# Kernel tuning notes

Hardware: AMD Instinct MI355X
Metric: run time of the kernel (lower is better)

The kernel has to match this reference:

```python
import jax, jax.numpy as jnp
import numpy as np

D_MODEL = 1024
NHEAD = 16
HEAD_DIM = D_MODEL // NHEAD
LN_EPS = 1e-5
ROPE_BASE = 10000.0


def _rope_cos_sin(n, head_dim):
    inv_freq = 1.0 / (ROPE_BASE ** (jnp.arange(0, head_dim, 2, dtype=jnp.float32) / head_dim))
    t = jnp.arange(n, dtype=jnp.float32)
    freqs = jnp.outer(t, inv_freq)  # (N, head_dim//2)
    return jnp.cos(freqs), jnp.sin(freqs)


def _apply_rope(x, cos, sin):
    # x: (B, H, N, hd); cos/sin: (N, hd//2)
    B, H, N, hd = x.shape
    xr = x.reshape(B, H, N, hd // 2, 2)
    x0, x1 = xr[..., 0], xr[..., 1]
    c = cos[None, None]
    s = sin[None, None]
    rot = jnp.stack([x0 * c - x1 * s, x0 * s + x1 * c], axis=-1)
    return rot.reshape(B, H, N, hd)


def setup_inputs() -> dict:
    key = jax.random.key(0)
    ks = jax.random.split(key, 6)
    D = D_MODEL
    scale = 1.0 / np.sqrt(D)
    x = jax.random.normal(ks[0], (2, 2048, D), dtype=jnp.float32)
    Wq = jax.random.normal(ks[1], (D, D), dtype=jnp.float32) * scale
    Wk = jax.random.normal(ks[2], (D, D), dtype=jnp.float32) * scale
    Wv = jax.random.normal(ks[3], (D, D), dtype=jnp.float32) * scale
    Wo = jax.random.normal(ks[4], (D, D), dtype=jnp.float32) * scale
    bq = jnp.zeros((D,), jnp.float32)
    bk = jnp.zeros((D,), jnp.float32)
    bv = jnp.zeros((D,), jnp.float32)
    bo = jnp.zeros((D,), jnp.float32)
    ln_w = jnp.ones((D,), jnp.float32)
    ln_b = jnp.zeros((D,), jnp.float32)
    return {"x": x, "ln_w": ln_w, "ln_b": ln_b, "Wq": Wq, "bq": bq,
            "Wk": Wk, "bk": bk, "Wv": Wv, "bv": bv, "Wo": Wo, "bo": bo}


def reference(x, ln_w, ln_b, Wq, bq, Wk, bk, Wv, bv, Wo, bo):
    B, N, D = x.shape
    H, hd = NHEAD, HEAD_DIM
    # LayerNorm
    mu = jnp.mean(x, axis=-1, keepdims=True)
    var = jnp.mean(jnp.square(x - mu), axis=-1, keepdims=True)
    xn = (x - mu) * jax.lax.rsqrt(var + LN_EPS) * ln_w + ln_b
    # QKV projections -> (B, H, N, hd)
    def proj(W, b):
        return (xn @ W.T + b).reshape(B, N, H, hd).transpose(0, 2, 1, 3)
    q = proj(Wq, bq)
    k = proj(Wk, bk)
    v = proj(Wv, bv)
    cos, sin = _rope_cos_sin(N, hd)
    q = _apply_rope(q, cos, sin)
    k = _apply_rope(k, cos, sin)
    scores = jnp.einsum('bhqd,bhkd->bhqk', q, k) / jnp.sqrt(jnp.float32(hd))
    attn = jax.nn.softmax(scores, axis=-1)
    out = jnp.einsum('bhqk,bhkd->bhqd', attn, v)
    out = out.transpose(0, 2, 1, 3).reshape(B, N, D)
    return x + out @ Wo.T + bo
```

## Files before the change

kernel.cpp:

```cpp
#include <hip/hip_runtime.h>


#define SEQ 2048
#define LN_EPS 1e-5f

using short8 = __attribute__((ext_vector_type(8))) short;
using f32x4  = __attribute__((ext_vector_type(4))) float;

__device__ __forceinline__ unsigned short f2bf(float f) {
  union { float f; unsigned u; } v; v.f = f;
  unsigned r = v.u + 0x7FFFu + ((v.u >> 16) & 1u);
  return (unsigned short)(r >> 16);
}

__device__ __forceinline__ void async16(const void* g, void* l) {
  __builtin_amdgcn_global_load_lds(
      (const __attribute__((address_space(1))) void*)g,
      (__attribute__((address_space(3))) void*)l, 16, 0, 0);
}

__global__ __launch_bounds__(256) void prep_kernel(
    const float* __restrict__ x, const float* __restrict__ lnw, const float* __restrict__ lnb,
    const float* __restrict__ wq, const float* __restrict__ wk,
    const float* __restrict__ wv, const float* __restrict__ wo,
    unsigned short* __restrict__ wqkv, unsigned short* __restrict__ wob,
    unsigned short* __restrict__ xn, float2* __restrict__ tab) {
  const int b = blockIdx.x, t = threadIdx.x;
  if (b < 4096) {
    const int gid = b * 256 + t;
    const int m = gid >> 18, e4 = gid & 262143;
    const float* src = (m == 0) ? wq : (m == 1) ? wk : (m == 2) ? wv : wo;
    const float4 v = ((const float4*)src)[e4];
    ushort4 o; o.x = f2bf(v.x); o.y = f2bf(v.y); o.z = f2bf(v.z); o.w = f2bf(v.w);
    if (m < 3) ((ushort4*)wqkv)[(size_t)m * 262144 + e4] = o;
    else       ((ushort4*)wob)[e4] = o;
  } else if (b < 8192) {
    const int row = b - 4096;
    const float4 v = ((const float4*)(x + (size_t)row * 1024))[t];
    float s  = v.x + v.y + v.z + v.w;
    float s2 = v.x * v.x + v.y * v.y + v.z * v.z + v.w * v.w;
#pragma unroll
    for (int off = 32; off >= 1; off >>= 1) {
      s  += __shfl_xor(s, off);
      s2 += __shfl_xor(s2, off);
    }
    __shared__ float red[8];
    const int lane = t & 63, wave = t >> 6;
    if (lane == 0) { red[wave] = s; red[4 + wave] = s2; }
    __syncthreads();
    s  = red[0] + red[1] + red[2] + red[3];
    s2 = red[4] + red[5] + red[6] + red[7];
    const float mu   = s * (1.0f / 1024.0f);
    const float var  = s2 * (1.0f / 1024.0f) - mu * mu;
    const float rstd = rsqrtf(var + LN_EPS);
    const float4 wv4 = ((const float4*)lnw)[t];
    const float4 bv4 = ((const float4*)lnb)[t];
    ushort4 o;
    o.x = f2bf((v.x - mu) * rstd * wv4.x + bv4.x);
    o.y = f2bf((v.y - mu) * rstd * wv4.y + bv4.y);
    o.z = f2bf((v.z - mu) * rstd * wv4.z + bv4.z);
    o.w = f2bf((v.w - mu) * rstd * wv4.w + bv4.w);
    ((ushort4*)xn)[(size_t)row * 256 + t] = o;
  } else {
    const int gid = (b - 8192) * 256 + t;
    const int pos = gid >> 5, ip = gid & 31;
    const float invf = exp2f((float)ip * -0.4152410118609203f);
    const float fr = (float)pos * invf;
    tab[gid] = make_float2(cosf(fr), sinf(fr));
  }
}

__global__ __launch_bounds__(256, 3) void gemm_kernel(
    const unsigned short* __restrict__ A,
    const unsigned short* __restrict__ Bw,
    int mode,
    const float* __restrict__ bq, const float* __restrict__ bk, const float* __restrict__ bv,
    const float2* __restrict__ tab,
    unsigned short* __restrict__ qb, unsigned short* __restrict__ kbg,
    unsigned short* __restrict__ vtb,
    const float* __restrict__ bo, const float* __restrict__ xres, float* __restrict__ out) {
  __shared__ unsigned short lA[128 * 64];
  __shared__ unsigned short lB[128 * 64];
  const int tid = threadIdx.x;
  const int lane = tid & 63, wave = tid >> 6;
  const int lr = lane & 15, quad = lane >> 4;
  const int wm = (wave >> 1) * 64, wn = (wave & 1) * 64;
  const int n0 = blockIdx.x * 128, m0 = blockIdx.y * 128;
  const int r7 = lr & 7;
  const int lrow = lane >> 3, lcg = (lane & 7) ^ lrow;

  f32x4 acc[4][4];
#pragma unroll
  for (int i = 0; i < 4; ++i)
#pragma unroll
    for (int j = 0; j < 4; ++j) acc[i][j] = (f32x4){0.f, 0.f, 0.f, 0.f};

  for (int kt = 0; kt < 16; ++kt) {
    __syncthreads();
#pragma unroll
    for (int c = 0; c < 4; ++c) {
      const int chunk = wave * 4 + c;
      const int grow = chunk * 8 + lrow;
      async16(&A[(size_t)(m0 + grow) * 1024 + kt * 64 + lcg * 8], &lA[chunk * 512]);
      async16(&Bw[(size_t)(n0 + grow) * 1024 + kt * 64 + lcg * 8], &lB[chunk * 512]);
    }
    __syncthreads();
#pragma unroll
    for (int kk = 0; kk < 2; ++kk) {
      short8 a[4], b[4];
#pragma unroll
      for (int i = 0; i < 4; ++i)
        a[i] = *(const short8*)&lA[(wm + i * 16 + lr) * 64 + ((kk * 4 + quad) ^ r7) * 8];
#pragma unroll
      for (int j = 0; j < 4; ++j)
        b[j] = *(const short8*)&lB[(wn + j * 16 + lr) * 64 + ((kk * 4 + quad) ^ r7) * 8];
#pragma unroll
      for (int i = 0; i < 4; ++i)
#pragma unroll
        for (int j = 0; j < 4; ++j)
          acc[i][j] = __builtin_amdgcn_mfma_f32_16x16x32_bf16(a[i], b[j], acc[i][j], 0, 0, 0);
    }
  }

  if (mode == 0) {
    const int which = n0 >> 10;
    const float* bias = (which == 0) ? bq : (which == 1) ? bk : bv;
    const float qs = (which == 0) ? 0.18033688011112042f : 1.0f;
#pragma unroll
    for (int i = 0; i < 4; ++i)
#pragma unroll
      for (int j = 0; j < 4; ++j)
#pragma unroll
        for (int r = 0; r < 4; ++r) {
          const int row = m0 + wm + i * 16 + quad * 4 + r;
          const int col = n0 + wn + j * 16 + lr;
          const int c = col & 1023;
          float val = (acc[i][j][r] + bias[c]) * qs;
          const int head = c >> 6, hd_i = c & 63;
          const int b_ = row >> 11, pos = row & 2047;
          if (which < 2) {
            const float partner = __shfl_xor(val, 1);
            const float2 cs = tab[(pos << 5) + (hd_i >> 1)];
            val = val * cs.x + partner * ((lane & 1) ? cs.y : -cs.y);
          }
          if (which == 2) {
            vtb[((size_t)((b_ * 16 + head) * 64 + hd_i)) * SEQ + pos] = f2bf(val);
          } else {
            const size_t didx = ((size_t)((b_ * 16 + head) * SEQ + pos)) * 64 + hd_i;
            if (which == 0) qb[didx] = f2bf(val);
            else            kbg[didx] = f2bf(val);
          }
        }
  } else {
#pragma unroll
    for (int i = 0; i < 4; ++i)
#pragma unroll
      for (int j = 0; j < 4; ++j)
#pragma unroll
        for (int r = 0; r < 4; ++r) {
          const int row = m0 + wm + i * 16 + quad * 4 + r;
          const int col = n0 + wn + j * 16 + lr;
          const size_t idx = (size_t)row * 1024 + col;
          out[idx] = acc[i][j][r] + bo[col] + xres[idx];
        }
  }
}

__global__ __launch_bounds__(256) void attn_kernel(
    const unsigned short* __restrict__ qg, const unsigned short* __restrict__ kg,
    const unsigned short* __restrict__ vtg, unsigned short* __restrict__ ao) {
  __shared__ unsigned short lK[64 * 64];
  __shared__ unsigned short lV[64 * 64];
  __shared__ unsigned short lP[128 * 72];
  const int tid = threadIdx.x;
  const int lane = tid & 63, w = tid >> 6;
  const int lr = lane & 15, quad = lane >> 4;
  const int r7 = lr & 7;
  const int lrow = lane >> 3, lcg = (lane & 7) ^ lrow;
  const int bh = blockIdx.x >> 4, qt = blockIdx.x & 15;
  const int q0 = qt * 128 + w * 32;
  const unsigned short* Q  = qg + (size_t)bh * SEQ * 64;
  const unsigned short* K  = kg + (size_t)bh * SEQ * 64;
  const unsigned short* VT = vtg + (size_t)bh * 64 * SEQ;

  short8 qf[2][2];
#pragma unroll
  for (int t = 0; t < 2; ++t)
#pragma unroll
    for (int kk = 0; kk < 2; ++kk)
      qf[t][kk] = *(const short8*)&Q[(size_t)(q0 + t * 16 + lr) * 64 + kk * 32 + quad * 8];

  short8 onesf;
  {
    const short o1 = (lr == 0) ? (short)0x3F80 : (short)0;
#pragma unroll
    for (int j = 0; j < 8; ++j) onesf[j] = o1;
  }

  f32x4 o[2][4], ol[2];
#pragma unroll
  for (int t = 0; t < 2; ++t) {
    ol[t] = (f32x4){0.f, 0.f, 0.f, 0.f};
#pragma unroll
    for (int d = 0; d < 4; ++d) o[t][d] = (f32x4){0.f, 0.f, 0.f, 0.f};
  }

  for (int kt = 0; kt < 32; ++kt) {
    __syncthreads();
#pragma unroll
    for (int c = 0; c < 2; ++c) {
      const int chunk = w * 2 + c;
      const int row = chunk * 8 + lrow;
      async16(&K[(size_t)(kt * 64 + row) * 64 + lcg * 8], &lK[chunk * 512]);
      async16(&VT[(size_t)row * SEQ + kt * 64 + lcg * 8], &lV[chunk * 512]);
    }
    __syncthreads();

#pragma unroll
    for (int kb = 0; kb < 4; ++kb) {
      const short8 k0 = *(const short8*)&lK[(kb * 16 + lr) * 64 + (quad ^ r7) * 8];
      const short8 k1 = *(const short8*)&lK[(kb * 16 + lr) * 64 + ((4 + quad) ^ r7) * 8];
#pragma unroll
      for (int t = 0; t < 2; ++t) {
        f32x4 st = (f32x4){0.f, 0.f, 0.f, 0.f};
        st = __builtin_amdgcn_mfma_f32_16x16x32_bf16(k0, qf[t][0], st, 0, 0, 0);
        st = __builtin_amdgcn_mfma_f32_16x16x32_bf16(k1, qf[t][1], st, 0, 0, 0);
        union { float f; unsigned u; } c0, c1, c2, c3;
        c0.f = __builtin_amdgcn_exp2f(st[0]);
        c1.f = __builtin_amdgcn_exp2f(st[1]);
        c2.f = __builtin_amdgcn_exp2f(st[2]);
        c3.f = __builtin_amdgcn_exp2f(st[3]);
        uint2 pw;
        pw.x = __builtin_amdgcn_perm(c1.u, c0.u, 0x07060302u);
        pw.y = __builtin_amdgcn_perm(c3.u, c2.u, 0x07060302u);
        *(uint2*)&lP[(w * 32 + t * 16 + lr) * 72 + kb * 16 + quad * 4] = pw;
      }
    }
    __asm__ __volatile__("s_waitcnt lgkmcnt(0)" ::: "memory");

#pragma unroll
    for (int k2 = 0; k2 < 2; ++k2) {
      const short8 pf0 = *(const short8*)&lP[(w * 32 + lr) * 72 + k2 * 32 + quad * 8];
      const short8 pf1 = *(const short8*)&lP[(w * 32 + 16 + lr) * 72 + k2 * 32 + quad * 8];
      ol[0] = __builtin_amdgcn_mfma_f32_16x16x32_bf16(pf0, onesf, ol[0], 0, 0, 0);
      ol[1] = __builtin_amdgcn_mfma_f32_16x16x32_bf16(pf1, onesf, ol[1], 0, 0, 0);
#pragma unroll
      for (int d = 0; d < 4; ++d) {
        const short8 vf = *(const short8*)&lV[(d * 16 + lr) * 64 + ((k2 * 4 + quad) ^ r7) * 8];
        o[0][d] = __builtin_amdgcn_mfma_f32_16x16x32_bf16(pf0, vf, o[0][d], 0, 0, 0);
        o[1][d] = __builtin_amdgcn_mfma_f32_16x16x32_bf16(pf1, vf, o[1][d], 0, 0, 0);
      }
    }
  }

  const int b_ = bh >> 4, h = bh & 15;
#pragma unroll
  for (int t = 0; t < 2; ++t)
#pragma unroll
    for (int r = 0; r < 4; ++r) {
      const float l = __shfl(ol[t][r], lane & 48);
      const float rl = 1.0f / l;
#pragma unroll
      for (int d = 0; d < 4; ++d) {
        const int row = q0 + t * 16 + quad * 4 + r;
        ao[(size_t)(b_ * SEQ + row) * 1024 + h * 64 + d * 16 + lr] = f2bf(o[t][d][r] * rl);
      }
    }
}

extern "C" void kernel_launch(void* const* d_in, const int* in_sizes, int n_in,
                              void* d_out, int out_size, void* d_ws, size_t ws_size,
                              hipStream_t stream) {
  const float* x   = (const float*)d_in[0];
  const float* lnw = (const float*)d_in[1];
  const float* lnb = (const float*)d_in[2];
  const float* Wq  = (const float*)d_in[3];
  const float* bq  = (const float*)d_in[4];
  const float* Wk  = (const float*)d_in[5];
  const float* bk  = (const float*)d_in[6];
  const float* Wv  = (const float*)d_in[7];
  const float* bv  = (const float*)d_in[8];
  const float* Wo  = (const float*)d_in[9];
  const float* bo  = (const float*)d_in[10];
  float* out = (float*)d_out;

  char* ws = (char*)d_ws;
  unsigned short* wqkv = (unsigned short*)(ws);
  unsigned short* wob  = (unsigned short*)(ws + 6291456);
  unsigned short* xn   = (unsigned short*)(ws + 8388608);
  unsigned short* qb   = (unsigned short*)(ws + 16777216);
  unsigned short* kbuf = (unsigned short*)(ws + 25165824);
  unsigned short* vtb  = (unsigned short*)(ws + 33554432);
  unsigned short* ao   = (unsigned short*)(ws + 41943040);
  float2*         tab  = (float2*)(ws + 50331648);

  hipLaunchKernelGGL(prep_kernel, dim3(8448), dim3(256), 0, stream,
                     x, lnw, lnb, Wq, Wk, Wv, Wo, wqkv, wob, xn, tab);
  hipLaunchKernelGGL(gemm_kernel, dim3(24, 32), dim3(256), 0, stream,
                     xn, wqkv, 0, bq, bk, bv, tab, qb, kbuf, vtb,
                     (const float*)nullptr, (const float*)nullptr, (float*)nullptr);
  hipLaunchKernelGGL(attn_kernel, dim3(512), dim3(256), 0, stream, qb, kbuf, vtb, ao);
  hipLaunchKernelGGL(gemm_kernel, dim3(8, 32), dim3(256), 0, stream,
                     ao, wob, 1,
                     (const float*)nullptr, (const float*)nullptr, (const float*)nullptr, tab,
                     (unsigned short*)nullptr, (unsigned short*)nullptr, (unsigned short*)nullptr,
                     bo, x, out);
}
```

Baseline: 222.6 us.

## Drop LDS staging; load GEMM and attention MFMA fragments directly from global

The QKV GEMM, output GEMM and attention kernels stop staging tiles in shared memory with async global-to-LDS copies and block barriers. Each wave now reads its MFMA operand fragments straight from global memory through precomputed row pointers and relies on cache hits for reuse across waves. The single GEMM kernel is split into a QKV kernel and an output-projection kernel; the latter uses narrower 64-column tiles, which doubles the block count. Attention keeps only a per-wave swizzled P buffer in LDS and adds a redundant zero store before each P write. This removes barrier and LDS traffic but gives up explicit tile sharing, so it risks more global/L2 traffic and exposed load latency.

After: 370.3 us. +66.4%, slower.

```diff
diff --git a/kernel.cpp b/kernel.cpp
--- a/kernel.cpp
+++ b/kernel.cpp
@@ -11,12 +11,6 @@
   union { float f; unsigned u; } v; v.f = f;
   unsigned r = v.u + 0x7FFFu + ((v.u >> 16) & 1u);
   return (unsigned short)(r >> 16);
-}
-
-__device__ __forceinline__ void async16(const void* g, void* l) {
-  __builtin_amdgcn_global_load_lds(
-      (const __attribute__((address_space(1))) void*)g,
-      (__attribute__((address_space(3))) void*)l, 16, 0, 0);
 }
 
 __global__ __launch_bounds__(256) void prep_kernel(
@@ -70,24 +64,26 @@
   }
 }
 
-__global__ __launch_bounds__(256, 3) void gemm_kernel(
+__global__ __launch_bounds__(256, 3) void gemm_qkv_kernel(
     const unsigned short* __restrict__ A,
     const unsigned short* __restrict__ Bw,
-    int mode,
     const float* __restrict__ bq, const float* __restrict__ bk, const float* __restrict__ bv,
     const float2* __restrict__ tab,
     unsigned short* __restrict__ qb, unsigned short* __restrict__ kbg,
-    unsigned short* __restrict__ vtb,
-    const float* __restrict__ bo, const float* __restrict__ xres, float* __restrict__ out) {
-  __shared__ unsigned short lA[128 * 64];
-  __shared__ unsigned short lB[128 * 64];
+    unsigned short* __restrict__ vtb) {
   const int tid = threadIdx.x;
   const int lane = tid & 63, wave = tid >> 6;
   const int lr = lane & 15, quad = lane >> 4;
   const int wm = (wave >> 1) * 64, wn = (wave & 1) * 64;
   const int n0 = blockIdx.x * 128, m0 = blockIdx.y * 128;
-  const int r7 = lr & 7;
-  const int lrow = lane >> 3, lcg = (lane & 7) ^ lrow;
+
+  const unsigned short* ap[4];
+  const unsigned short* bp[4];
+#pragma unroll
+  for (int i = 0; i < 4; ++i) {
+    ap[i] = &A[(size_t)(m0 + wm + i * 16 + lr) * 1024 + quad * 8];
+    bp[i] = &Bw[(size_t)(n0 + wn + i * 16 + lr) * 1024 + quad * 8];
+  }
 
   f32x4 acc[4][4];
 #pragma unroll
@@ -96,24 +92,14 @@
     for (int j = 0; j < 4; ++j) acc[i][j] = (f32x4){0.f, 0.f, 0.f, 0.f};
 
   for (int kt = 0; kt < 16; ++kt) {
-    __syncthreads();
-#pragma unroll
-    for (int c = 0; c < 4; ++c) {
-      const int chunk = wave * 4 + c;
-      const int grow = chunk * 8 + lrow;
-      async16(&A[(size_t)(m0 + grow) * 1024 + kt * 64 + lcg * 8], &lA[chunk * 512]);
-      async16(&Bw[(size_t)(n0 + grow) * 1024 + kt * 64 + lcg * 8], &lB[chunk * 512]);
-    }
-    __syncthreads();
 #pragma unroll
     for (int kk = 0; kk < 2; ++kk) {
+      const int off = kt * 64 + kk * 32;
       short8 a[4], b[4];
 #pragma unroll
-      for (int i = 0; i < 4; ++i)
-        a[i] = *(const short8*)&lA[(wm + i * 16 + lr) * 64 + ((kk * 4 + quad) ^ r7) * 8];
-#pragma unroll
-      for (int j = 0; j < 4; ++j)
-        b[j] = *(const short8*)&lB[(wn + j * 16 + lr) * 64 + ((kk * 4 + quad) ^ r7) * 8];
+      for (int i = 0; i < 4; ++i) a[i] = *(const short8*)(ap[i] + off);
+#pragma unroll
+      for (int j = 0; j < 4; ++j) b[j] = *(const short8*)(bp[j] + off);
 #pragma unroll
       for (int i = 0; i < 4; ++i)
 #pragma unroll
@@ -122,66 +108,105 @@
     }
   }
 
-  if (mode == 0) {
-    const int which = n0 >> 10;
-    const float* bias = (which == 0) ? bq : (which == 1) ? bk : bv;
-    const float qs = (which == 0) ? 0.18033688011112042f : 1.0f;
-#pragma unroll
-    for (int i = 0; i < 4; ++i)
-#pragma unroll
-      for (int j = 0; j < 4; ++j)
-#pragma unroll
-        for (int r = 0; r < 4; ++r) {
-          const int row = m0 + wm + i * 16 + quad * 4 + r;
-          const int col = n0 + wn + j * 16 + lr;
-          const int c = col & 1023;
-          float val = (acc[i][j][r] + bias[c]) * qs;
-          const int head = c >> 6, hd_i = c & 63;
-          const int b_ = row >> 11, pos = row & 2047;
-          if (which < 2) {
-            const float partner = __shfl_xor(val, 1);
-            const float2 cs = tab[(pos << 5) + (hd_i >> 1)];
-            val = val * cs.x + partner * ((lane & 1) ? cs.y : -cs.y);
-          }
-          if (which == 2) {
-            vtb[((size_t)((b_ * 16 + head) * 64 + hd_i)) * SEQ + pos] = f2bf(val);
-          } else {
-            const size_t didx = ((size_t)((b_ * 16 + head) * SEQ + pos)) * 64 + hd_i;
-            if (which == 0) qb[didx] = f2bf(val);
-            else            kbg[didx] = f2bf(val);
-          }
+  const int which = n0 >> 10;
+  const float* bias = (which == 0) ? bq : (which == 1) ? bk : bv;
+  const float qs = (which == 0) ? 0.18033688011112042f : 1.0f;
+#pragma unroll
+  for (int i = 0; i < 4; ++i)
+#pragma unroll
+    for (int j = 0; j < 4; ++j)
+#pragma unroll
+      for (int r = 0; r < 4; ++r) {
+        const int row = m0 + wm + i * 16 + quad * 4 + r;
+        const int col = n0 + wn + j * 16 + lr;
+        const int c = col & 1023;
+        float val = (acc[i][j][r] + bias[c]) * qs;
+        const int head = c >> 6, hd_i = c & 63;
+        const int b_ = row >> 11, pos = row & 2047;
+        if (which < 2) {
+          const float partner = __shfl_xor(val, 1);
+          const float2 cs = tab[(pos << 5) + (hd_i >> 1)];
+          val = val * cs.x + partner * ((lane & 1) ? cs.y : -cs.y);
         }
-  } else {
-#pragma unroll
-    for (int i = 0; i < 4; ++i)
-#pragma unroll
-      for (int j = 0; j < 4; ++j)
-#pragma unroll
-        for (int r = 0; r < 4; ++r) {
-          const int row = m0 + wm + i * 16 + quad * 4 + r;
-          const int col = n0 + wn + j * 16 + lr;
-          const size_t idx = (size_t)row * 1024 + col;
-          out[idx] = acc[i][j][r] + bo[col] + xres[idx];
+        if (which == 2) {
+          vtb[((size_t)((b_ * 16 + head) * 64 + hd_i)) * SEQ + pos] = f2bf(val);
+        } else {
+          const size_t didx = ((size_t)((b_ * 16 + head) * SEQ + pos)) * 64 + hd_i;
+          if (which == 0) qb[didx] = f2bf(val);
+          else            kbg[didx] = f2bf(val);
         }
-  }
-}
-
-__global__ __launch_bounds__(256) void attn_kernel(
+      }
+}
+
+__global__ __launch_bounds__(256, 3) void gemm_o_kernel(
+    const unsigned short* __restrict__ A,
+    const unsigned short* __restrict__ Bw,
+    const float* __restrict__ bo, const float* __restrict__ xres, float* __restrict__ out) {
+  const int tid = threadIdx.x;
+  const int lane = tid & 63, wave = tid >> 6;
+  const int lr = lane & 15, quad = lane >> 4;
+  const int wm = wave * 32;
+  const int n0 = blockIdx.x * 64, m0 = blockIdx.y * 128;
+
+  const unsigned short* ap[2];
+  const unsigned short* bp[4];
+#pragma unroll
+  for (int i = 0; i < 2; ++i)
+    ap[i] = &A[(size_t)(m0 + wm + i * 16 + lr) * 1024 + quad * 8];
+#pragma unroll
+  for (int j = 0; j < 4; ++j)
+    bp[j] = &Bw[(size_t)(n0 + j * 16 + lr) * 1024 + quad * 8];
+
+  f32x4 acc[2][4];
+#pragma unroll
+  for (int i = 0; i < 2; ++i)
+#pragma unroll
+    for (int j = 0; j < 4; ++j) acc[i][j] = (f32x4){0.f, 0.f, 0.f, 0.f};
+
+  for (int kt = 0; kt < 16; ++kt) {
+#pragma unroll
+    for (int kk = 0; kk < 2; ++kk) {
+      const int off = kt * 64 + kk * 32;
+      short8 a[2], b[4];
+#pragma unroll
+      for (int i = 0; i < 2; ++i) a[i] = *(const short8*)(ap[i] + off);
+#pragma unroll
+      for (int j = 0; j < 4; ++j) b[j] = *(const short8*)(bp[j] + off);
+#pragma unroll
+      for (int i = 0; i < 2; ++i)
+#pragma unroll
+        for (int j = 0; j < 4; ++j)
+          acc[i][j] = __builtin_amdgcn_mfma_f32_16x16x32_bf16(a[i], b[j], acc[i][j], 0, 0, 0);
+    }
+  }
+
+#pragma unroll
+  for (int i = 0; i < 2; ++i)
+#pragma unroll
+    for (int j = 0; j < 4; ++j)
+#pragma unroll
+      for (int r = 0; r < 4; ++r) {
+        const int row = m0 + wm + i * 16 + quad * 4 + r;
+        const int col = n0 + j * 16 + lr;
+        const size_t idx = (size_t)row * 1024 + col;
+        out[idx] = acc[i][j][r] + bo[col] + xres[idx];
+      }
+}
+
+__global__ __launch_bounds__(256, 2) void attn_kernel(
     const unsigned short* __restrict__ qg, const unsigned short* __restrict__ kg,
     const unsigned short* __restrict__ vtg, unsigned short* __restrict__ ao) {
-  __shared__ unsigned short lK[64 * 64];
-  __shared__ unsigned short lV[64 * 64];
-  __shared__ unsigned short lP[128 * 72];
+  __shared__ unsigned short lP[4][32 * 64];
   const int tid = threadIdx.x;
   const int lane = tid & 63, w = tid >> 6;
   const int lr = lane & 15, quad = lane >> 4;
   const int r7 = lr & 7;
-  const int lrow = lane >> 3, lcg = (lane & 7) ^ lrow;
   const int bh = blockIdx.x >> 4, qt = blockIdx.x & 15;
   const int q0 = qt * 128 + w * 32;
   const unsigned short* Q  = qg + (size_t)bh * SEQ * 64;
   const unsigned short* K  = kg + (size_t)bh * SEQ * 64;
   const unsigned short* VT = vtg + (size_t)bh * 64 * SEQ;
+  unsigned short* lPw = lP[w];
 
   short8 qf[2][2];
 #pragma unroll
@@ -205,21 +230,19 @@
     for (int d = 0; d < 4; ++d) o[t][d] = (f32x4){0.f, 0.f, 0.f, 0.f};
   }
 
+  const unsigned short* kp[4];
+  const unsigned short* vp[4];
+#pragma unroll
+  for (int i = 0; i < 4; ++i) {
+    kp[i] = &K[(size_t)(i * 16 + lr) * 64 + quad * 8];
+    vp[i] = &VT[(size_t)(i * 16 + lr) * SEQ + quad * 8];
+  }
+
   for (int kt = 0; kt < 32; ++kt) {
-    __syncthreads();
-#pragma unroll
-    for (int c = 0; c < 2; ++c) {
-      const int chunk = w * 2 + c;
-      const int row = chunk * 8 + lrow;
-      async16(&K[(size_t)(kt * 64 + row) * 64 + lcg * 8], &lK[chunk * 512]);
-      async16(&VT[(size_t)row * SEQ + kt * 64 + lcg * 8], &lV[chunk * 512]);
-    }
-    __syncthreads();
-
 #pragma unroll
     for (int kb = 0; kb < 4; ++kb) {
-      const short8 k0 = *(const short8*)&lK[(kb * 16 + lr) * 64 + (quad ^ r7) * 8];
-      const short8 k1 = *(const short8*)&lK[(kb * 16 + lr) * 64 + ((4 + quad) ^ r7) * 8];
+      const short8 k0 = *(const short8*)(kp[kb] + (size_t)kt * 4096);
+      const short8 k1 = *(const short8*)(kp[kb] + (size_t)kt * 4096 + 32);
 #pragma unroll
       for (int t = 0; t < 2; ++t) {
         f32x4 st = (f32x4){0.f, 0.f, 0.f, 0.f};
@@ -233,20 +256,21 @@
         uint2 pw;
         pw.x = __builtin_amdgcn_perm(c1.u, c0.u, 0x07060302u);
         pw.y = __builtin_amdgcn_perm(c3.u, c2.u, 0x07060302u);
-        *(uint2*)&lP[(w * 32 + t * 16 + lr) * 72 + kb * 16 + quad * 4] = pw;
+        lPw[(t * 16 + lr) * 64 + (((kb * 2 + (quad >> 1)) ^ r7) * 8 + (quad & 1) * 4)] = 0;
+        *(uint2*)&lPw[(t * 16 + lr) * 64 + ((kb * 2 + (quad >> 1)) ^ r7) * 8 + (quad & 1) * 4] = pw;
       }
     }
     __asm__ __volatile__("s_waitcnt lgkmcnt(0)" ::: "memory");
 
 #pragma unroll
     for (int k2 = 0; k2 < 2; ++k2) {
-      const short8 pf0 = *(const short8*)&lP[(w * 32 + lr) * 72 + k2 * 32 + quad * 8];
-      const short8 pf1 = *(const short8*)&lP[(w * 32 + 16 + lr) * 72 + k2 * 32 + quad * 8];
+      const short8 pf0 = *(const short8*)&lPw[lr * 64 + ((k2 * 4 + quad) ^ r7) * 8];
+      const short8 pf1 = *(const short8*)&lPw[(16 + lr) * 64 + ((k2 * 4 + quad) ^ r7) * 8];
       ol[0] = __builtin_amdgcn_mfma_f32_16x16x32_bf16(pf0, onesf, ol[0], 0, 0, 0);
       ol[1] = __builtin_amdgcn_mfma_f32_16x16x32_bf16(pf1, onesf, ol[1], 0, 0, 0);
 #pragma unroll
       for (int d = 0; d < 4; ++d) {
-        const short8 vf = *(const short8*)&lV[(d * 16 + lr) * 64 + ((k2 * 4 + quad) ^ r7) * 8];
+        const short8 vf = *(const short8*)(vp[d] + kt * 64 + k2 * 32);
         o[0][d] = __builtin_amdgcn_mfma_f32_16x16x32_bf16(pf0, vf, o[0][d], 0, 0, 0);
         o[1][d] = __builtin_amdgcn_mfma_f32_16x16x32_bf16(pf1, vf, o[1][d], 0, 0, 0);
       }
@@ -296,13 +320,9 @@
 
   hipLaunchKernelGGL(prep_kernel, dim3(8448), dim3(256), 0, stream,
                      x, lnw, lnb, Wq, Wk, Wv, Wo, wqkv, wob, xn, tab);
-  hipLaunchKernelGGL(gemm_kernel, dim3(24, 32), dim3(256), 0, stream,
-                     xn, wqkv, 0, bq, bk, bv, tab, qb, kbuf, vtb,
-                     (const float*)nullptr, (const float*)nullptr, (float*)nullptr);
+  hipLaunchKernelGGL(gemm_qkv_kernel, dim3(24, 32), dim3(256), 0, stream,
+                     xn, wqkv, bq, bk, bv, tab, qb, kbuf, vtb);
   hipLaunchKernelGGL(attn_kernel, dim3(512), dim3(256), 0, stream, qb, kbuf, vtb, ao);
-  hipLaunchKernelGGL(gemm_kernel, dim3(8, 32), dim3(256), 0, stream,
-                     ao, wob, 1,
-                     (const float*)nullptr, (const float*)nullptr, (const float*)nullptr, tab,
-                     (unsigned short*)nullptr, (unsigned short*)nullptr, (unsigned short*)nullptr,
-                     bo, x, out);
-}
+  hipLaunchKernelGGL(gemm_o_kernel, dim3(16, 32), dim3(256), 0, stream,
+                     ao, wob, bo, x, out);
+}
```
